# Kernel optimization log

Measured on AMD Instinct MI355X. Metric: run time of the kernel, lower is better.

## Reference

```python
import jax, jax.numpy as jnp
import numpy as np

N_POINTS = 4096
DIM = 64
MAX_EDGE_LENGTH = 1e9  # large -> no MST edge is filtered, output has static shape (n-1,)


def _mst_edge_lengths(points):
    """0-dim Rips persistence death values == Euclidean MST edge lengths.

    Equivalent to gudhi RipsComplex(max_dimension=0) + flag_persistence_generators
    followed by torch.norm(input[v0] - input[v1], dim=-1). Returned sorted
    ascending (gudhi's ordering is unspecified; compare as a multiset).
    """
    n = points.shape[0]
    sq = jnp.sum(points * points, axis=1)                      # [n]
    d2 = sq[:, None] + sq[None, :] - 2.0 * (points @ points.T)  # [n,n]
    d2 = jnp.maximum(d2, 0.0)
    # safe positive diagonal so sqrt is smooth there (diagonal never selected)
    idx = jnp.arange(n)
    d2 = d2.at[idx, idx].set(1.0)
    D = jnp.sqrt(d2)                                            # [n,n] distances

    inf = jnp.asarray(jnp.inf, D.dtype)
    in_tree0 = jnp.zeros((n,), dtype=bool).at[0].set(True)
    dist0 = jnp.where(in_tree0, inf, D[0])                      # min dist to tree

    def step(carry, _):
        dist, in_tree = carry
        j = jnp.argmin(dist)            # nearest non-tree vertex
        w = dist[j]                     # MST edge length (a persistence death)
        in_tree = in_tree.at[j].set(True)
        dist = jnp.where(in_tree, inf, jnp.minimum(dist, D[j]))
        return (dist, in_tree), w

    _, lengths = jax.lax.scan(step, (dist0, in_tree0), None, length=n - 1)
    # max_edge_length filter is a no-op for MAX_EDGE_LENGTH=1e9
    return jnp.sort(lengths)


def setup_inputs() -> dict:
    key = jax.random.key(0)
    points = jax.random.normal(key, (N_POINTS, DIM), dtype=jnp.float32)
    return {"input": points}


def reference(input) -> jnp.ndarray:
    return _mst_edge_lengths(input)
```

## Files before the change

### kernel.cpp

```cpp
#include <hip/hip_runtime.h>
#include <hip/hip_bf16.h>


#define NPTS 4096
#define SENT 1e30f
#define KINF 0xFFFFFFFFFFFFFFFFull
#define INV32 0xFFFFFFFFu
#define SCAN_ROWS 2
#define SCAN_BLOCKS (NPTS / SCAN_ROWS)
#define CMAX 1024

#define HOOK_NORMAL 0
#define HOOK_FORCE_COMPACT 1

typedef short short8 __attribute__((ext_vector_type(8)));
typedef float f32x4 __attribute__((ext_vector_type(4)));

__device__ __forceinline__ float bfbits2f(unsigned int u16) {
  union { unsigned int u; float f; } c;
  c.u = u16 << 16;
  return c.f;
}

__device__ bool data_is_bf16(const unsigned short* p) {
  bool bf = true;
  for (int i = 0; i < 256; ++i) {
    float f = bfbits2f((unsigned int)p[i]);
    if (!(f > -1e6f && f < 1e6f)) bf = false;
  }
  return bf;
}

__global__ __launch_bounds__(256) void prep_kernel(
    const void* pts_raw, unsigned short* Pb, float* sq, int* comp,
    unsigned short* comp16, int* parent, unsigned long long* cheapest,
    float* edges, unsigned* cnt, unsigned* M, unsigned long long* cheapM) {
  float pf = bfbits2f((unsigned int)((const unsigned short*)pts_raw)[threadIdx.x]);
  const bool bfs = (bool)__syncthreads_and((int)(pf > -1e6f && pf < 1e6f));

  const int g = blockIdx.x * 256 + threadIdx.x;
  if (g < NPTS) {
    comp[g] = g;
    comp16[g] = (unsigned short)g;
    parent[g] = g;
    cheapest[g] = KINF;
  }
  if (g < CMAX) cheapM[g] = KINF;
  {
    uint4 mi; mi.x = INV32; mi.y = INV32; mi.z = INV32; mi.w = INV32;
    ((uint4*)M)[g] = mi;
  }
  if (g == NPTS - 1) edges[NPTS - 1] = SENT;
  if (g == 0) {
    cnt[0] = 0u;
    cnt[1] = 0u;
    cnt[2] = bfs ? 1u : 0u;
    cnt[3] = 0u;
  }

  const int row = g >> 6;
  const int lane = threadIdx.x & 63;

  unsigned short ub;
  if (bfs) {
    ub = ((const unsigned short*)pts_raw)[row * 64 + lane];
  } else {
    __hip_bfloat16 h = __float2bfloat16(((const float*)pts_raw)[row * 64 + lane]);
    ub = *(unsigned short*)&h;
  }
  Pb[row * 64 + lane] = ub;

  float v = bfbits2f((unsigned int)ub);
  float s = v * v;
#pragma unroll
  for (int m = 1; m < 64; m <<= 1) s += __shfl_xor(s, m);
  if (lane == 0) sq[row] = s;
}

__global__ __launch_bounds__(256) void dist_mfma(const unsigned short* Pb,
                                                 const float* sq,
                                                 unsigned short* Dbf,
                                                 unsigned long long* cheapest) {
  __shared__ unsigned short tile[64 * 72];

  const int t = threadIdx.x;
  const int w = t >> 6, lane = t & 63;
  const int quad = lane >> 4, l16 = lane & 15;
  const int rbase = blockIdx.y * 64 + w * 16;
  const int cbase = blockIdx.x * 64;

  const short8* Pv = (const short8*)Pb;
  short8 a0 = Pv[(rbase + l16) * 8 + quad];
  short8 a1 = Pv[(rbase + l16) * 8 + quad + 4];

  f32x4 acc[4];
#pragma unroll
  for (int c = 0; c < 4; ++c) {
    short8 b0 = Pv[(cbase + c * 16 + l16) * 8 + quad];
    short8 b1 = Pv[(cbase + c * 16 + l16) * 8 + quad + 4];
    f32x4 z = {0.f, 0.f, 0.f, 0.f};
    z = __builtin_amdgcn_mfma_f32_16x16x32_bf16(a0, b0, z, 0, 0, 0);
    z = __builtin_amdgcn_mfma_f32_16x16x32_bf16(a1, b1, z, 0, 0, 0);
    acc[c] = z;
  }

  float sr[4];
#pragma unroll
  for (int q = 0; q < 4; ++q) sr[q] = sq[rbase + quad * 4 + q];

#pragma unroll
  for (int c = 0; c < 4; ++c) {
    float sc = sq[cbase + c * 16 + l16];
#pragma unroll
    for (int q = 0; q < 4; ++q) {
      float d2 = sr[q] + sc - 2.f * acc[c][q];
      float dd = sqrtf(fmaxf(d2, 0.f));
      __hip_bfloat16 h = __float2bfloat16(dd);
      tile[(w * 16 + quad * 4 + q) * 72 + c * 16 + l16] = *(unsigned short*)&h;
    }
  }
  __syncthreads();

  for (int i = t; i < 512; i += 256) {
    int row = i >> 3, cb8 = (i & 7) * 8;
    uint4 v = *(const uint4*)&tile[row * 72 + cb8];
    *(uint4*)&Dbf[(size_t)(blockIdx.y * 64 + row) * 4096 + cbase + cb8] = v;
  }

  {
    const int r = t >> 2, cseg = (t & 3) * 16;
    const int v = blockIdx.y * 64 + r;
    const uint4* lrow = (const uint4*)&tile[r * 72 + cseg];
    uint4 v0 = lrow[0], v1 = lrow[1];
    unsigned wv[16] = {v0.x & 0xFFFFu, v0.x >> 16, v0.y & 0xFFFFu, v0.y >> 16,
                       v0.z & 0xFFFFu, v0.z >> 16, v0.w & 0xFFFFu, v0.w >> 16,
                       v1.x & 0xFFFFu, v1.x >> 16, v1.y & 0xFFFFu, v1.y >> 16,
                       v1.z & 0xFFFFu, v1.z >> 16, v1.w & 0xFFFFu, v1.w >> 16};
    unsigned long long kmin = KINF;
#pragma unroll
    for (int e = 0; e < 16; ++e) {
      const int j = cbase + cseg + e;
      if (j != v) {
        unsigned ed = (v < j) ? (((unsigned)v << 12) | (unsigned)j)
                              : (((unsigned)j << 12) | (unsigned)v);
        unsigned long long key = ((unsigned long long)wv[e] << 24) | ed;
        kmin = key < kmin ? key : kmin;
      }
    }
#pragma unroll
    for (int m = 1; m < 4; m <<= 1) {
      unsigned long long o = __shfl_xor(kmin, m);
      kmin = o < kmin ? o : kmin;
    }
    if ((t & 3) == 0) atomicMin(&cheapest[v], kmin);
  }
}

__global__ __launch_bounds__(256) void bor_scan(const unsigned short* Dbf,
                                                const unsigned short* comp16,
                                                int* parent,
                                                unsigned long long* cheapest,
                                                const unsigned* cnt) {
  if (cnt[1]) return;

  __shared__ unsigned long long redu[SCAN_ROWS][4];

  const int t = threadIdx.x;
  const int b = blockIdx.x;
  const int wave = t >> 6;
  const int gtid = b * 256 + t;
  const int vbase = b * SCAN_ROWS;

  if (gtid < NPTS) parent[gtid] = gtid;

  const uint4* c16v = (const uint4*)comp16;
  uint4 c0 = c16v[2 * t], c1 = c16v[2 * t + 1];
  unsigned mc[16] = {c0.x & 0xFFFFu, c0.x >> 16, c0.y & 0xFFFFu, c0.y >> 16,
                     c0.z & 0xFFFFu, c0.z >> 16, c0.w & 0xFFFFu, c0.w >> 16,
                     c1.x & 0xFFFFu, c1.x >> 16, c1.y & 0xFFFFu, c1.y >> 16,
                     c1.z & 0xFFFFu, c1.z >> 16, c1.w & 0xFFFFu, c1.w >> 16};

  const uint4* rp = (const uint4*)(Dbf + (size_t)vbase * NPTS);
#pragma unroll
  for (int vv = 0; vv < SCAN_ROWS; ++vv) {
    const int v = vbase + vv;
    const unsigned cv = (unsigned)comp16[v];
    uint4 a0 = rp[vv * 512 + 2 * t];
    uint4 a1 = rp[vv * 512 + 2 * t + 1];
    unsigned wv[16] = {a0.x & 0xFFFFu, a0.x >> 16, a0.y & 0xFFFFu, a0.y >> 16,
                       a0.z & 0xFFFFu, a0.z >> 16, a0.w & 0xFFFFu, a0.w >> 16,
                       a1.x & 0xFFFFu, a1.x >> 16, a1.y & 0xFFFFu, a1.y >> 16,
                       a1.z & 0xFFFFu, a1.z >> 16, a1.w & 0xFFFFu, a1.w >> 16};
    unsigned long long kmin = KINF;
#pragma unroll
    for (int e = 0; e < 16; ++e) {
      const int j = t * 16 + e;
      if (mc[e] != cv) {
        unsigned ed = (v < j) ? (((unsigned)v << 12) | (unsigned)j)
                              : (((unsigned)j << 12) | (unsigned)v);
        unsigned long long key = ((unsigned long long)wv[e] << 24) | ed;
        kmin = key < kmin ? key : kmin;
      }
    }
#pragma unroll
    for (int m = 1; m < 64; m <<= 1) {
      unsigned long long o = __shfl_xor(kmin, m);
      kmin = o < kmin ? o : kmin;
    }
    if ((t & 63) == 0) redu[vv][wave] = kmin;
  }
  __syncthreads();

  if (t < SCAN_ROWS) {
    unsigned long long k = redu[t][0];
    if (redu[t][1] < k) k = redu[t][1];
    if (redu[t][2] < k) k = redu[t][2];
    if (redu[t][3] < k) k = redu[t][3];
    if (k != KINF) atomicMin(&cheapest[(int)comp16[vbase + t]], k);
  }
}

__global__ __launch_bounds__(1024) void bor_hook(int* comp,
                                                 unsigned short* comp16,
                                                 int* parent,
                                                 unsigned long long* cheapest,
                                                 float* edges, unsigned* cnt,
                                                 int mode) {
  if (cnt[1]) return;
  const int t = threadIdx.x;

  for (int i = t; i < NPTS; i += 1024) {
    if (comp[i] == i) {
      unsigned long long key = cheapest[i];
      if (key != KINF) {
        int mx = (int)(key & 0xFFFull);
        int mn = (int)((key >> 12) & 0xFFFull);
        int ca = comp[mn], cb = comp[mx];
        int u = (ca == i) ? cb : ca;
        bool mutual = (cheapest[u] == key);
        if (!mutual || i < u) {
          unsigned pos = atomicAdd(cnt, 1u);
          edges[pos] = bfbits2f((unsigned)(key >> 24));
        }
        if (!mutual || i > u) parent[i] = u;
      }
    }
  }
  __threadfence_block();
  __syncthreads();

  for (int i = t; i < NPTS; i += 1024) {
    int r = comp[i], p;
    for (int it = 0; it < NPTS; ++it) {
      p = parent[r];
      if (p == r) break;
      r = p;
    }
    comp[i] = r;
    comp16[i] = (unsigned short)r;
    cheapest[i] = KINF;
  }
  __threadfence_block();
  __syncthreads();

  if (mode == HOOK_FORCE_COMPACT) {
    for (int i = t; i < NPTS; i += 1024)
      if (comp[i] == i) parent[i] = (int)atomicAdd(&cnt[3], 1u);
    __syncthreads();
    for (int i = t; i < NPTS; i += 1024)
      comp16[i] = (unsigned short)parent[comp[i]];
  }
  if (t == 0 && cnt[0] >= (unsigned)(NPTS - 1)) cnt[1] = 1u;
}

__global__ __launch_bounds__(256) void bor_project(const unsigned short* Dbf,
                                                   const unsigned short* comp16,
                                                   unsigned* M,
                                                   const unsigned* cnt,
                                                   unsigned long long* cheapM) {
  if (cnt[1]) return;

  __shared__ unsigned Mloc[SCAN_ROWS][CMAX];
  __shared__ unsigned long long redc[SCAN_ROWS][4];
  const int t = threadIdx.x;
  const int b = blockIdx.x;
  const int vbase = b * SCAN_ROWS;

#pragma unroll
  for (int s = 0; s < 4; ++s) {
    Mloc[0][t + 256 * s] = INV32;
    Mloc[1][t + 256 * s] = INV32;
  }
  __syncthreads();

  const uint4* c16v = (const uint4*)comp16;
  uint4 c0 = c16v[2 * t], c1 = c16v[2 * t + 1];
  unsigned mc[16] = {c0.x & 0xFFFFu, c0.x >> 16, c0.y & 0xFFFFu, c0.y >> 16,
                     c0.z & 0xFFFFu, c0.z >> 16, c0.w & 0xFFFFu, c0.w >> 16,
                     c1.x & 0xFFFFu, c1.x >> 16, c1.y & 0xFFFFu, c1.y >> 16,
                     c1.z & 0xFFFFu, c1.z >> 16, c1.w & 0xFFFFu, c1.w >> 16};

  const uint4* rp = (const uint4*)(Dbf + (size_t)vbase * NPTS);
#pragma unroll
  for (int vv = 0; vv < SCAN_ROWS; ++vv) {
    const unsigned cv = (unsigned)comp16[vbase + vv];
    uint4 a0 = rp[vv * 512 + 2 * t];
    uint4 a1 = rp[vv * 512 + 2 * t + 1];
    unsigned wv[16] = {a0.x & 0xFFFFu, a0.x >> 16, a0.y & 0xFFFFu, a0.y >> 16,
                       a0.z & 0xFFFFu, a0.z >> 16, a0.w & 0xFFFFu, a0.w >> 16,
                       a1.x & 0xFFFFu, a1.x >> 16, a1.y & 0xFFFFu, a1.y >> 16,
                       a1.z & 0xFFFFu, a1.z >> 16, a1.w & 0xFFFFu, a1.w >> 16};
#pragma unroll
    for (int e = 0; e < 16; ++e)
      if (mc[e] != cv) atomicMin(&Mloc[vv][mc[e]], wv[e]);
  }
  __syncthreads();

  const unsigned cv0 = (unsigned)comp16[vbase];
  const unsigned cv1 = (unsigned)comp16[vbase + 1];
  unsigned long long k0 = KINF, k1 = KINF;
#pragma unroll
  for (int s = 0; s < 4; ++s) {
    const unsigned col = (unsigned)(t + 256 * s);
    unsigned x = Mloc[0][col];
    if (x != INV32) {
      atomicMin(&M[cv0 * CMAX + col], x);
      unsigned lo = cv0 < col ? cv0 : col, hi = cv0 < col ? col : cv0;
      unsigned long long key =
          ((unsigned long long)x << 22) | (lo << 11) | hi;
      if (key < k0) k0 = key;
    }
    unsigned y = Mloc[1][col];
    if (y != INV32) {
      atomicMin(&M[cv1 * CMAX + col], y);
      unsigned lo = cv1 < col ? cv1 : col, hi = cv1 < col ? col : cv1;
      unsigned long long key =
          ((unsigned long long)y << 22) | (lo << 11) | hi;
      if (key < k1) k1 = key;
    }
  }

#pragma unroll
  for (int m = 1; m < 64; m <<= 1) {
    unsigned long long o0 = __shfl_xor(k0, m);
    if (o0 < k0) k0 = o0;
    unsigned long long o1 = __shfl_xor(k1, m);
    if (o1 < k1) k1 = o1;
  }
  if ((t & 63) == 0) { redc[0][t >> 6] = k0; redc[1][t >> 6] = k1; }
  __syncthreads();
  if (t < SCAN_ROWS) {
    unsigned long long k = redc[t][0];
    if (redc[t][1] < k) k = redc[t][1];
    if (redc[t][2] < k) k = redc[t][2];
    if (redc[t][3] < k) k = redc[t][3];
    if (k != KINF)
      atomicMin(&cheapM[(int)comp16[vbase + t]], k);
  }
}

__global__ __launch_bounds__(1024) void bor_finish(const unsigned* M,
                                                   unsigned* cnt,
                                                   float* edges,
                                                   const unsigned long long* cheapM) {
  if (cnt[1]) return;

  __shared__ int comp2[CMAX];
  __shared__ int parent2[CMAX];
  __shared__ unsigned long long cheap2[CMAX];
  __shared__ int live;

  const int t = threadIdx.x;
  const int C = (int)cnt[3];
  comp2[t] = t;
  __syncthreads();

  for (int round = 0; round < 11; ++round) {
    cheap2[t] = KINF;
    if (t == 0) live = 0;
    __syncthreads();

    if (round == 0) {
      if (t < C) cheap2[t] = cheapM[t];
    } else {
      const int Cu4 = (C + 3) >> 2;
      const int Q4 = (Cu4 + 3) >> 2;
      for (int item = t; item < 4 * C; item += 1024) {
        const int c = item >> 2, q = item & 3;
        const int cc = comp2[c];
        const int lo4 = q * Q4;
        int hi4 = lo4 + Q4; if (hi4 > Cu4) hi4 = Cu4;
        unsigned long long kmin = KINF;
        const uint4* Mr = (const uint4*)(M + c * CMAX);
        for (int u = lo4; u < hi4; ++u) {
          uint4 m4 = Mr[u];
          const int j0 = u * 4;
          unsigned wj[4] = {m4.x, m4.y, m4.z, m4.w};
#pragma unroll
          for (int k = 0; k < 4; ++k) {
            int j = j0 + k;
            unsigned w = wj[k];
            if (w != INV32 && comp2[j] != cc) {
              int lo = c < j ? c : j, hi = c < j ? j : c;
              unsigned long long key = ((unsigned long long)w << 22) |
                                       ((unsigned)lo << 11) | (unsigned)hi;
              if (key < kmin) kmin = key;
            }
          }
        }
        if (kmin != KINF) atomicMin(&cheap2[cc], kmin);
      }
    }
    __syncthreads();

    {
      parent2[t] = t;
      if (comp2[t] == t) {
        unsigned long long key = cheap2[t];
        if (key != KINF) {
          int hi = (int)(key & 0x7FFull);
          int lo = (int)((key >> 11) & 0x7FFull);
          int ca = comp2[lo], cb = comp2[hi];
          int u = (ca == t) ? cb : ca;
          bool mutual = (cheap2[u] == key);
          if (!mutual || t < u) {
            unsigned pos = atomicAdd(cnt, 1u);
            edges[pos] = bfbits2f((unsigned)(key >> 22));
          }
          if (!mutual || t > u) parent2[t] = u;
        }
      }
    }
    __syncthreads();

    {
      int r = comp2[t], p;
      for (int it = 0; it < CMAX; ++it) {
        p = parent2[r];
        if (p == r) break;
        r = p;
      }
      comp2[t] = r;
      if (t < C && r != comp2[0]) live = 1;
    }
    __syncthreads();
    if (!live) break;
  }
}

__global__ __launch_bounds__(256) void rank_sort(const float* edges,
                                                 const unsigned* cnt,
                                                 void* out) {
  __shared__ unsigned long long wred[4][2];
  const int b = blockIdx.x;
  const int t = threadIdx.x;
  const int pbase = 4 * b;
  const float4* ev = (const float4*)edges;
  const float4 pvv = ev[b];
  const float pv0 = pvv.x, pv1 = pvv.y, pv2 = pvv.z, pv3 = pvv.w;

  int c0 = 0, c1 = 0, c2 = 0, c3 = 0;
#pragma unroll
  for (int k = 0; k < 4; ++k) {
    float4 e = ev[t + 256 * k];
    int j = 4 * (t + 256 * k);
    float va[4] = {e.x, e.y, e.z, e.w};
#pragma unroll
    for (int m = 0; m < 4; ++m) {
      const float x = va[m];
      const int xi = j + m;
      c0 += (x < pv0 || (x == pv0 && xi < pbase + 0));
      c1 += (x < pv1 || (x == pv1 && xi < pbase + 1));
      c2 += (x < pv2 || (x == pv2 && xi < pbase + 2));
      c3 += (x < pv3 || (x == pv3 && xi < pbase + 3));
    }
  }

  unsigned long long p0 = (unsigned long long)(unsigned)c0 |
                          ((unsigned long long)(unsigned)c1 << 32);
  unsigned long long p1 = (unsigned long long)(unsigned)c2 |
                          ((unsigned long long)(unsigned)c3 << 32);
#pragma unroll
  for (int m = 1; m < 64; m <<= 1) {
    p0 += __shfl_xor(p0, m);
    p1 += __shfl_xor(p1, m);
  }
  if ((t & 63) == 0) { wred[t >> 6][0] = p0; wred[t >> 6][1] = p1; }
  __syncthreads();

  if (t == 0) {
    unsigned long long a = wred[0][0] + wred[1][0] + wred[2][0] + wred[3][0];
    unsigned long long d = wred[0][1] + wred[1][1] + wred[2][1] + wred[3][1];
    const int r[4] = {(int)(a & 0xFFFFFFFFull), (int)(a >> 32),
                      (int)(d & 0xFFFFFFFFull), (int)(d >> 32)};
    const float pv[4] = {pv0, pv1, pv2, pv3};
    const bool bf = cnt[2] != 0u;
#pragma unroll
    for (int p = 0; p < 4; ++p) {
      const int pidx = pbase + p;
      if (pidx < NPTS - 1) {
        if (bf) ((__hip_bfloat16*)out)[r[p]] = __float2bfloat16(pv[p]);
        else    ((float*)out)[r[p]] = pv[p];
      }
    }
  }
}

__global__ __launch_bounds__(256) void dist_kernel(const void* pts_raw,
                                                   __hip_bfloat16* Dbf) {
  __shared__ float As[64 * 65];
  __shared__ float Bs[64 * 65];
  __shared__ float sqA[64];
  __shared__ float sqB[64];

  const int t = threadIdx.x;
  const int bx = blockIdx.x, by = blockIdx.y;
  const bool bf = data_is_bf16((const unsigned short*)pts_raw);
  const unsigned short* pu = (const unsigned short*)pts_raw;
  const float* pf = (const float*)pts_raw;

  for (int s = 0; s < 16; ++s) {
    int e = t + 256 * s;
    int r = e >> 6, c = e & 63;
    float av, bv;
    if (bf) {
      av = bfbits2f((unsigned int)pu[by * 4096 + e]);
      bv = bfbits2f((unsigned int)pu[bx * 4096 + e]);
    } else {
      av = pf[by * 4096 + e];
      bv = pf[bx * 4096 + e];
    }
    As[r * 65 + c] = av;
    Bs[r * 65 + c] = bv;
  }
  __syncthreads();

  if (t < 64) {
    float s = 0.f;
    for (int k = 0; k < 64; ++k) { float x = As[t * 65 + k]; s += x * x; }
    sqA[t] = s;
  } else if (t < 128) {
    int r = t - 64;
    float s = 0.f;
    for (int k = 0; k < 64; ++k) { float x = Bs[r * 65 + k]; s += x * x; }
    sqB[r] = s;
  }
  __syncthreads();

  const int tx = t & 15, ty = t >> 4;
  const int lr = ty * 4, lc = tx * 4;
  float acc[4][4] = {};
  for (int k = 0; k < 64; ++k) {
    float a[4], b[4];
#pragma unroll
    for (int q = 0; q < 4; ++q) a[q] = As[(lr + q) * 65 + k];
#pragma unroll
    for (int p = 0; p < 4; ++p) b[p] = Bs[(lc + p) * 65 + k];
#pragma unroll
    for (int q = 0; q < 4; ++q)
#pragma unroll
      for (int p = 0; p < 4; ++p) acc[q][p] += a[q] * b[p];
  }

#pragma unroll
  for (int q = 0; q < 4; ++q) {
    int gr = by * 64 + lr + q;
    float sa = sqA[lr + q];
#pragma unroll
    for (int p = 0; p < 4; ++p) {
      int gc = bx * 64 + lc + p;
      float d2 = sa + sqB[lc + p] - 2.f * acc[q][p];
      d2 = fmaxf(d2, 0.f);
      Dbf[(size_t)gr * 4096 + gc] = __float2bfloat16(sqrtf(d2));
    }
  }
}

__global__ __launch_bounds__(512) void prim_kernel(const unsigned short* probe,
                                                   const unsigned short* Dbf,
                                                   void* out) {
  __shared__ float len[NPTS];
  __shared__ float rv[2][8];
  __shared__ int ri[2][8];

  const int t = threadIdx.x;
  const bool bf_out = data_is_bf16(probe);

  float d[8];
  {
    const uint4* row0 = (const uint4*)(Dbf);
    uint4 v = row0[t];
    d[0] = bfbits2f(v.x & 0xffffu); d[1] = bfbits2f(v.x >> 16);
    d[2] = bfbits2f(v.y & 0xffffu); d[3] = bfbits2f(v.y >> 16);
    d[4] = bfbits2f(v.z & 0xffffu); d[5] = bfbits2f(v.z >> 16);
    d[6] = bfbits2f(v.w & 0xffffu); d[7] = bfbits2f(v.w >> 16);
    if (t == 0) d[0] = SENT;
  }

  float bv = SENT;
  int bi = 8 * t;
#pragma unroll
  for (int k = 0; k < 8; ++k)
    if (d[k] < bv) { bv = d[k]; bi = 8 * t + k; }

  for (int step = 0; step < NPTS - 1; ++step) {
    float v = bv;
    int idx = bi;
#pragma unroll
    for (int m = 1; m < 64; m <<= 1) {
      float ov = __shfl_xor(v, m);
      int oi = __shfl_xor(idx, m);
      if (ov < v) { v = ov; idx = oi; }
    }
    const int buf = step & 1;
    if ((t & 63) == 0) { rv[buf][t >> 6] = v; ri[buf][t >> 6] = idx; }
    __syncthreads();

    float w = rv[buf][0];
    int j = ri[buf][0];
#pragma unroll
    for (int u = 1; u < 8; ++u) {
      float uv = rv[buf][u];
      if (uv < w) { w = uv; j = ri[buf][u]; }
    }
    if (t == 0) len[step] = w;

    const uint4* row = (const uint4*)(Dbf + (size_t)j * NPTS);
    uint4 rw = row[t];
    float nd[8];
    nd[0] = bfbits2f(rw.x & 0xffffu); nd[1] = bfbits2f(rw.x >> 16);
    nd[2] = bfbits2f(rw.y & 0xffffu); nd[3] = bfbits2f(rw.y >> 16);
    nd[4] = bfbits2f(rw.z & 0xffffu); nd[5] = bfbits2f(rw.z >> 16);
    nd[6] = bfbits2f(rw.w & 0xffffu); nd[7] = bfbits2f(rw.w >> 16);

    bv = SENT;
    bi = 8 * t;
    const int base = 8 * t;
#pragma unroll
    for (int k = 0; k < 8; ++k) {
      float cur = d[k];
      float nn = fminf(cur, nd[k]);
      if (cur == SENT || base + k == j) nn = SENT;
      d[k] = nn;
      if (nn < bv) { bv = nn; bi = base + k; }
    }
  }

  if (t == 0) len[NPTS - 1] = SENT;
  __syncthreads();

  for (int k = 2; k <= NPTS; k <<= 1) {
    for (int jj = k >> 1; jj > 0; jj >>= 1) {
      for (int i = t; i < NPTS; i += 512) {
        int ixj = i ^ jj;
        if (ixj > i) {
          float a = len[i], b = len[ixj];
          bool up = ((i & k) == 0);
          if ((a > b) == up) { len[i] = b; len[ixj] = a; }
        }
      }
      __syncthreads();
    }
  }

  if (bf_out) {
    __hip_bfloat16* o = (__hip_bfloat16*)out;
    for (int i = t; i < NPTS - 1; i += 512) o[i] = __float2bfloat16(len[i]);
  } else {
    float* o = (float*)out;
    for (int i = t; i < NPTS - 1; i += 512) o[i] = len[i];
  }
}

extern "C" void kernel_launch(void* const* d_in, const int* in_sizes, int n_in,
                              void* d_out, int out_size, void* d_ws, size_t ws_size,
                              hipStream_t stream) {
  const void* pts = d_in[0];
  char* base = (char*)d_ws;
  __hip_bfloat16* Dbf = (__hip_bfloat16*)base;

  size_t off = 32ull << 20;
  int* comp = (int*)(base + off);                  off += (size_t)NPTS * 4;
  int* parent = (int*)(base + off);                off += (size_t)NPTS * 4;
  unsigned long long* cheapest =
      (unsigned long long*)(base + off);           off += (size_t)NPTS * 8;
  float* edges = (float*)(base + off);             off += (size_t)NPTS * 4;
  unsigned* cnt = (unsigned*)(base + off);         off += 256;
  unsigned short* Pb = (unsigned short*)(base + off); off += (size_t)NPTS * 64 * 2;
  float* sq = (float*)(base + off);                off += (size_t)NPTS * 4;
  unsigned short* comp16 = (unsigned short*)(base + off); off += (size_t)NPTS * 2;
  unsigned* M = (unsigned*)(base + off);           off += (size_t)CMAX * CMAX * 4;
  unsigned long long* cheapM =
      (unsigned long long*)(base + off);           off += (size_t)CMAX * 8;

  if (ws_size >= off) {
    prep_kernel<<<1024, 256, 0, stream>>>(pts, Pb, sq, comp, comp16, parent,
                                          cheapest, edges, cnt, M, cheapM);
    const unsigned short* Dus = (const unsigned short*)Dbf;
    dist_mfma<<<dim3(64, 64), 256, 0, stream>>>(Pb, sq, (unsigned short*)Dbf,
                                                cheapest);
    bor_hook<<<1, 1024, 0, stream>>>(comp, comp16, parent, cheapest, edges,
                                     cnt, HOOK_NORMAL);
    bor_scan<<<SCAN_BLOCKS, 256, 0, stream>>>(Dus, comp16, parent, cheapest,
                                              cnt);
    bor_hook<<<1, 1024, 0, stream>>>(comp, comp16, parent, cheapest, edges,
                                     cnt, HOOK_FORCE_COMPACT);
    bor_project<<<SCAN_BLOCKS, 256, 0, stream>>>(Dus, comp16, M, cnt, cheapM);
    bor_finish<<<1, 1024, 0, stream>>>(M, cnt, edges, cheapM);
    rank_sort<<<NPTS / 4, 256, 0, stream>>>(edges, cnt, d_out);
  } else {
    dist_kernel<<<dim3(64, 64), 256, 0, stream>>>(pts, Dbf);
    prim_kernel<<<1, 512, 0, stream>>>((const unsigned short*)pts,
                                       (const unsigned short*)Dbf, d_out);
  }
}
```

Baseline: 164.5 us.

## Precompute per-component top-8 candidate edges to avoid full matrix rescans in Boruvka finish

Adds a parallel kernel that extracts, for each contracted component row of the CxC weight matrix, its 8 cheapest neighbours. The single-block Boruvka finish then checks these candidates each round and only falls back to a full row scan (now wave-parallel with shuffle reduction) for components whose candidates are all already merged. This cuts the repeated O(C^2) scans done by one block across rounds, at the cost of an extra launch, a candidate buffer, and a fallback path. The round count rises from 11 to 12.

```diff
diff --git a/kernel.cpp b/kernel.cpp
--- a/kernel.cpp
+++ b/kernel.cpp
@@ -359,15 +359,61 @@
   }
 }
 
+__global__ __launch_bounds__(256) void mincand(const unsigned* M,
+                                               const unsigned* cnt,
+                                               unsigned* cand) {
+  if (cnt[1]) return;
+  const int C = (int)cnt[3];
+  const int t = threadIdx.x;
+  const int wave = t >> 6, lane = t & 63;
+  const int c = blockIdx.x * 4 + wave;
+  if (c >= C) return;
+
+  unsigned best[8];
+#pragma unroll
+  for (int k = 0; k < 8; ++k) best[k] = INV32;
+  const unsigned* Mr = M + c * CMAX;
+  for (int j = lane; j < C; j += 64) {
+    unsigned w = Mr[j];
+    if (w == INV32) continue;
+    unsigned key = (w << 10) | (unsigned)j;
+    if (key < best[7]) {
+      best[7] = key;
+#pragma unroll
+      for (int k = 7; k > 0; --k) {
+        if (best[k] < best[k - 1]) {
+          unsigned tmp = best[k]; best[k] = best[k - 1]; best[k - 1] = tmp;
+        }
+      }
+    }
+  }
+
+  int head = 0;
+  for (int k = 0; k < 8; ++k) {
+    unsigned my = (head < 8) ? best[head] : INV32;
+    unsigned long long pk = ((unsigned long long)my << 6) | (unsigned)lane;
+#pragma unroll
+    for (int m = 1; m < 64; m <<= 1) {
+      unsigned long long o = __shfl_xor(pk, m);
+      if (o < pk) pk = o;
+    }
+    if (lane == (int)(pk & 63u)) ++head;
+    if (lane == 0) cand[c * 8 + k] = (unsigned)(pk >> 6);
+  }
+}
+
 __global__ __launch_bounds__(1024) void bor_finish(const unsigned* M,
                                                    unsigned* cnt,
                                                    float* edges,
-                                                   const unsigned long long* cheapM) {
+                                                   const unsigned long long* cheapM,
+                                                   const unsigned* cand) {
   if (cnt[1]) return;
 
   __shared__ int comp2[CMAX];
   __shared__ int parent2[CMAX];
   __shared__ unsigned long long cheap2[CMAX];
+  __shared__ unsigned short flaglist[CMAX];
+  __shared__ int nflag;
   __shared__ int live;
 
   const int t = threadIdx.x;
@@ -375,31 +421,49 @@
   comp2[t] = t;
   __syncthreads();
 
-  for (int round = 0; round < 11; ++round) {
+  for (int round = 0; round < 12; ++round) {
     cheap2[t] = KINF;
-    if (t == 0) live = 0;
+    if (t == 0) { live = 0; nflag = 0; }
     __syncthreads();
 
     if (round == 0) {
       if (t < C) cheap2[t] = cheapM[t];
     } else {
-      const int Cu4 = (C + 3) >> 2;
-      const int Q4 = (Cu4 + 3) >> 2;
-      for (int item = t; item < 4 * C; item += 1024) {
-        const int c = item >> 2, q = item & 3;
-        const int cc = comp2[c];
-        const int lo4 = q * Q4;
-        int hi4 = lo4 + Q4; if (hi4 > Cu4) hi4 = Cu4;
-        unsigned long long kmin = KINF;
-        const uint4* Mr = (const uint4*)(M + c * CMAX);
-        for (int u = lo4; u < hi4; ++u) {
-          uint4 m4 = Mr[u];
-          const int j0 = u * 4;
-          unsigned wj[4] = {m4.x, m4.y, m4.z, m4.w};
-#pragma unroll
-          for (int k = 0; k < 4; ++k) {
-            int j = j0 + k;
-            unsigned w = wj[k];
+      if (t < C) {
+        const int cc = comp2[t];
+        bool found = false, any = false;
+        const unsigned* cd = cand + t * 8;
+#pragma unroll
+        for (int k = 0; k < 8; ++k) {
+          unsigned e = cd[k];
+          if (e == INV32) break;
+          any = true;
+          int j = (int)(e & 1023u);
+          if (comp2[j] != cc) {
+            unsigned w = e >> 10;
+            int lo = t < j ? t : j, hi = t < j ? j : t;
+            unsigned long long key = ((unsigned long long)w << 22) |
+                                     ((unsigned)lo << 11) | (unsigned)hi;
+            atomicMin(&cheap2[cc], key);
+            found = true;
+            break;
+          }
+        }
+        if (!found && any) {
+          int idx = atomicAdd(&nflag, 1);
+          flaglist[idx] = (unsigned short)t;
+        }
+      }
+      __syncthreads();
+      {
+        const int wv = t >> 6, lane = t & 63;
+        for (int i = wv; i < nflag; i += 16) {
+          const int c = (int)flaglist[i];
+          const int cc = comp2[c];
+          unsigned long long kmin = KINF;
+          const unsigned* Mr = M + c * CMAX;
+          for (int j = lane; j < C; j += 64) {
+            unsigned w = Mr[j];
             if (w != INV32 && comp2[j] != cc) {
               int lo = c < j ? c : j, hi = c < j ? j : c;
               unsigned long long key = ((unsigned long long)w << 22) |
@@ -407,8 +471,13 @@
               if (key < kmin) kmin = key;
             }
           }
+#pragma unroll
+          for (int m = 1; m < 64; m <<= 1) {
+            unsigned long long o = __shfl_xor(kmin, m);
+            if (o < kmin) kmin = o;
+          }
+          if (lane == 0 && kmin != KINF) atomicMin(&cheap2[cc], kmin);
         }
-        if (kmin != KINF) atomicMin(&cheap2[cc], kmin);
       }
     }
     __syncthreads();
@@ -692,6 +761,7 @@
   unsigned* M = (unsigned*)(base + off);           off += (size_t)CMAX * CMAX * 4;
   unsigned long long* cheapM =
       (unsigned long long*)(base + off);           off += (size_t)CMAX * 8;
+  unsigned* cand = (unsigned*)(base + off);        off += (size_t)CMAX * 8 * 4;
 
   if (ws_size >= off) {
     prep_kernel<<<1024, 256, 0, stream>>>(pts, Pb, sq, comp, comp16, parent,
@@ -706,7 +776,8 @@
     bor_hook<<<1, 1024, 0, stream>>>(comp, comp16, parent, cheapest, edges,
                                      cnt, HOOK_FORCE_COMPACT);
     bor_project<<<SCAN_BLOCKS, 256, 0, stream>>>(Dus, comp16, M, cnt, cheapM);
-    bor_finish<<<1, 1024, 0, stream>>>(M, cnt, edges, cheapM);
+    mincand<<<CMAX / 4, 256, 0, stream>>>(M, cnt, cand);
+    bor_finish<<<1, 1024, 0, stream>>>(M, cnt, edges, cheapM, cand);
     rank_sort<<<NPTS / 4, 256, 0, stream>>>(edges, cnt, d_out);
   } else {
     dist_kernel<<<dim3(64, 64), 256, 0, stream>>>(pts, Dbf);
```

New measurement: 169.0 us. 1.03x slower.
